# Performance work log

Measured on AMD Instinct MI355X. Metric: run time of the kernel, lower is better.

## Reference

```python
import jax, jax.numpy as jnp
import numpy as np

SEQ, B, V, E, H, L = 64, 64, 32000, 512, 512, 2


def setup_inputs() -> dict:
    key = jax.random.key(0)
    ks = jax.random.split(key, 12)
    k = float(np.sqrt(1.0 / H))
    u = lambda kk, shape, a, b: jax.random.uniform(kk, shape, jnp.float32, a, b)
    return {
        "inputs": jax.random.randint(ks[0], (SEQ, B), 0, V),          # [T, B] token ids
        "hidden": jnp.zeros((L, B, H), jnp.float32),                   # initial hidden
        "emb": u(ks[1], (V, E), -0.1, 0.1),                            # embedding table
        "Wr_w": u(ks[2], (L, H, E + H), -k, k),                        # reset gate [L,H,2H]
        "Wr_b": u(ks[3], (L, H), -k, k),
        "Wz_w": u(ks[4], (L, H, E + H), -k, k),                        # update gate
        "Wz_b": u(ks[5], (L, H), -k, k),
        "Wh_w": u(ks[6], (L, H, E + H), -k, k),                        # candidate
        "Wh_b": u(ks[7], (L, H), -k, k),
        "out_w": u(ks[8], (V, H), -0.1, 0.1),                          # output projection
        "out_b": jnp.zeros((V,), jnp.float32),
    }


def reference(inputs, hidden, emb, Wr_w, Wr_b, Wz_w, Wz_b, Wh_w, Wh_b, out_w, out_b):
    # GRU recurrence over time via lax.scan (dropout disabled: dp_keep_prob=1.0)
    def step(h, tok):
        x = emb[tok]  # [B, E]
        new_h = []
        for i in range(L):  # fixed small layer loop
            hi = h[i]  # [B, H]
            cat = jnp.concatenate([x, hi], axis=1)  # [B, E+H]
            r = jax.nn.sigmoid(cat @ Wr_w[i].T + Wr_b[i])
            z = jax.nn.sigmoid(cat @ Wz_w[i].T + Wz_b[i])
            h_hat = jnp.tanh(jnp.concatenate([x, r * hi], axis=1) @ Wh_w[i].T + Wh_b[i])
            x = (1.0 - z) * hi + z * h_hat  # next layer input / new hidden
            new_h.append(x)
        logits_t = x @ out_w.T + out_b  # [B, V]
        return jnp.stack(new_h), logits_t

    hidden_final, logits = jax.lax.scan(step, hidden, inputs)
    return logits, hidden_final  # [T,B,V], [L,B,H]
```

## Files before the change

kernel.cpp:

```cpp
#include <hip/hip_runtime.h>

constexpr int NT = 64;
constexpr int NB = 64;
constexpr int NV = 32000;
constexpr int NE = 512;
constexpr int NH = 512;
constexpr int NTILE = 32 * 250;

constexpr size_t SZ_OW  = (size_t)NV * NE;
constexpr size_t SZ_XE  = (size_t)NT * NB * NE;
constexpr size_t SZ_H   = (size_t)NB * NH;
constexpr size_t LOGITS = (size_t)NT * NB * NV;

typedef float f32x4 __attribute__((ext_vector_type(4)));
typedef int   i32x4 __attribute__((ext_vector_type(4)));
typedef short bf16x8 __attribute__((ext_vector_type(8)));
typedef short s16x4 __attribute__((ext_vector_type(4)));
typedef _Float16 f16x8 __attribute__((ext_vector_type(8)));

__device__ __forceinline__ unsigned short f2bf(float x) {
  unsigned u = __float_as_uint(x);
  u += 0x7FFFu + ((u >> 16) & 1u);
  return (unsigned short)(u >> 16);
}
__device__ __forceinline__ float bf2f(unsigned short s) {
  return __uint_as_float(((unsigned)s) << 16);
}
__device__ __forceinline__ void split2(float v, short* hi, short* lo) {
  unsigned short h = f2bf(v);
  *hi = (short)h;
  *lo = (short)f2bf(v - bf2f(h));
}
__device__ __forceinline__ f32x4 mma_bf16(bf16x8 a, bf16x8 b, f32x4 c) {
  return __builtin_amdgcn_mfma_f32_16x16x32_bf16(a, b, c, 0, 0, 0);
}
__device__ __forceinline__ f32x4 mma_f16(f16x8 a, f16x8 b, f32x4 c) {
  return __builtin_amdgcn_mfma_f32_16x16x32_f16(a, b, c, 0, 0, 0);
}

__device__ __forceinline__ void st_sc32u(unsigned* p, unsigned v) {
  asm volatile("global_store_dword %0, %1, off sc0 sc1" :: "v"(p), "v"(v) : "memory");
}
__device__ __forceinline__ void st_sc128(void* p, i32x4 v) {
  asm volatile("global_store_dwordx4 %0, %1, off sc0 sc1" :: "v"(p), "v"(v) : "memory");
}
__device__ __forceinline__ void st_nt(float* p, float v) {
  asm volatile("global_store_dword %0, %1, off nt" :: "v"(p), "v"(v) : "memory");
}
__device__ __forceinline__ unsigned ld_sc32u(const unsigned* p) {
  unsigned v;
  asm volatile("global_load_dword %0, %1, off sc0 sc1\n\ts_waitcnt vmcnt(0)"
               : "=v"(v) : "v"(p) : "memory");
  return v;
}

__device__ __forceinline__ void publish(unsigned* flags, int slot, unsigned val) {
  asm volatile("s_waitcnt vmcnt(0)" ::: "memory");
  __syncthreads();
  if (threadIdx.x == 0) st_sc32u(&flags[(size_t)slot * 32], val);
}

__global__ void k_prep(
    const float* __restrict__ outw, const int* __restrict__ toks,
    const float* __restrict__ emb, const float* __restrict__ hid,
    _Float16* OWf, short* XeHi, short* XeLo,
    short* X1Hi, short* X1Lo, short* h0Hi, short* h0Lo) {
  const size_t stride = (size_t)gridDim.x * blockDim.x;
  const size_t N1 = SZ_OW, N2 = N1 + SZ_XE, N3 = N2 + SZ_H, N4 = N3 + SZ_H;
  for (size_t x = (size_t)blockIdx.x * blockDim.x + threadIdx.x; x < N4; x += stride) {
    if (x < N1) {
      OWf[x] = (_Float16)outw[x];
    } else if (x < N2) {
      size_t p = x - N1;
      size_t r = p >> 9, c = p & 511u;
      int tok = toks[r];
      float v = emb[(size_t)tok * 512 + c];
      short hi, lo; split2(v, &hi, &lo);
      XeHi[p] = hi; XeLo[p] = lo;
    } else if (x < N3) {
      size_t p = x - N2;
      short hi, lo; split2(hid[p], &hi, &lo);
      h0Hi[p] = hi; h0Lo[p] = lo;
    } else {
      size_t p = x - N3;
      short hi, lo; split2(hid[SZ_H + p], &hi, &lo);
      X1Hi[p] = hi; X1Lo[p] = lo;
    }
  }
}

__device__ __forceinline__ void mmaP32(
    const short* __restrict__ aH, const short* __restrict__ aL, int base,
    const short* lsHi_, const short* lsLo_,
    f32x4 (&accH)[2], f32x4 (&accL)[2], int wave, int l15, int lq) {
  const int kq = wave >> 1, rhalf = wave & 1;
  const int r0 = rhalf * 16 + l15;
#pragma unroll
  for (int i = 0; i < 4; ++i) {
    const int ko = kq * 128 + i * 32 + lq * 8;
    const int kg = base + ko;
    const int e0 = (l15 * 1024 + kg) ^ ((l15 & 7) << 3);
    const int e1 = ((16 + l15) * 1024 + kg) ^ ((l15 & 7) << 3);
    bf16x8 bh0 = *(const bf16x8*)&lsHi_[e0];
    bf16x8 bl0 = *(const bf16x8*)&lsLo_[e0];
    bf16x8 bh1 = *(const bf16x8*)&lsHi_[e1];
    bf16x8 bl1 = *(const bf16x8*)&lsLo_[e1];
    bf16x8 ah = *(const bf16x8*)&aH[r0 * 512 + ko];
    bf16x8 al = *(const bf16x8*)&aL[r0 * 512 + ko];
    accH[0] = mma_bf16(ah, bh0, accH[0]);
    accH[1] = mma_bf16(ah, bh1, accH[1]);
    accL[0] = mma_bf16(al, bh0, accL[0]);
    accL[1] = mma_bf16(al, bh1, accL[1]);
    accL[0] = mma_bf16(ah, bl0, accL[0]);
    accL[1] = mma_bf16(ah, bl1, accL[1]);
  }
}
__device__ __forceinline__ void reduce4(float* lsRed_, f32x4 (&accH)[2], f32x4 (&accL)[2],
                                        f32x4 (&acc)[2], int wave, int l15, int lq) {
  const int kq = wave >> 1, rhalf = wave & 1;
  acc[0] = accH[0] + accL[0];
  acc[1] = accH[1] + accL[1];
  const int pos = l15 * 16 + lq * 4;
  if (kq) {
    *(f32x4*)&lsRed_[(((kq - 1) * 2 + rhalf) * 2 + 0) * 256 + pos] = acc[0];
    *(f32x4*)&lsRed_[(((kq - 1) * 2 + rhalf) * 2 + 1) * 256 + pos] = acc[1];
  }
  __syncthreads();
  if (!kq) {
#pragma unroll
    for (int s = 0; s < 3; ++s) {
      acc[0] += *(const f32x4*)&lsRed_[((s * 2 + rhalf) * 2 + 0) * 256 + pos];
      acc[1] += *(const f32x4*)&lsRed_[((s * 2 + rhalf) * 2 + 1) * 256 + pos];
    }
  }
  __syncthreads();
}

__device__ __forceinline__ void mmaD(
    const short* __restrict__ pAH, const short* __restrict__ pAL,
    int kloc0, int kkGlob0, const short* lsHi_, const short* lsLo_,
    f32x4 (&accH)[2], f32x4 (&accL)[2], int l15, int lq, int rhalf, int rowbase) {
  const int r0 = rowbase + rhalf * 16 + l15;
#pragma unroll 4
  for (int i = 0; i < 8; ++i) {
    const int kk = kkGlob0 + i * 32 + lq * 8;
    const int ka = kloc0 + i * 32 + lq * 8;
    const int e0 = (l15 * 1024 + kk) ^ ((l15 & 7) << 3);
    const int e1 = ((16 + l15) * 1024 + kk) ^ ((l15 & 7) << 3);
    bf16x8 bh0 = *(const bf16x8*)&lsHi_[e0];
    bf16x8 bl0 = *(const bf16x8*)&lsLo_[e0];
    bf16x8 bh1 = *(const bf16x8*)&lsHi_[e1];
    bf16x8 bl1 = *(const bf16x8*)&lsLo_[e1];
    bf16x8 ah = *(const bf16x8*)&pAH[r0 * 512 + ka];
    bf16x8 al = *(const bf16x8*)&pAL[r0 * 512 + ka];
    accH[0] = mma_bf16(ah, bh0, accH[0]);
    accH[1] = mma_bf16(ah, bh1, accH[1]);
    accL[0] = mma_bf16(al, bh0, accL[0]);
    accL[1] = mma_bf16(al, bh1, accL[1]);
    accL[0] = mma_bf16(ah, bl0, accL[0]);
    accL[1] = mma_bf16(ah, bl1, accL[1]);
  }
}
__device__ __forceinline__ void phaseD(
    const short* aLoH, const short* aLoL,
    const short* aHiH, const short* aHiL,
    const short* lsHi_, const short* lsLo_, float* lsRed_,
    f32x4 (&acc)[2], int wave, int l15, int lq, int rowbase) {
  const int khalf = wave >> 1, rhalf = wave & 1;
  f32x4 accH[2] = {}, accL[2] = {};
  const short* pAH = (khalf < 2) ? aLoH : aHiH;
  const short* pAL = (khalf < 2) ? aLoL : aHiL;
  mmaD(pAH, pAL, (khalf & 1) * 256, khalf * 256, lsHi_, lsLo_,
       accH, accL, l15, lq, rhalf, rowbase);
  acc[0] = accH[0] + accL[0];
  acc[1] = accH[1] + accL[1];
  const int pos = l15 * 16 + lq * 4;
  if (wave >= 2) {
    *(f32x4*)&lsRed_[((wave - 2) * 2 + 0) * 256 + pos] = acc[0];
    *(f32x4*)&lsRed_[((wave - 2) * 2 + 1) * 256 + pos] = acc[1];
  }
  __syncthreads();
  if (wave < 2) {
#pragma unroll
    for (int s = 0; s < 3; ++s) {
      const int slot = (wave & 1) + 2 * s;
      acc[0] += *(const f32x4*)&lsRed_[(slot * 2 + 0) * 256 + pos];
      acc[1] += *(const f32x4*)&lsRed_[(slot * 2 + 1) * 256 + pos];
    }
  }
  __syncthreads();
}

__device__ __forceinline__ void stage_weights(
    short* lsHi, short* lsLo, const float* srcBase0, const float* srcBase1,
    int jc, int tid) {
  for (int i = tid; i < 8192; i += 512) {
    const int j = i >> 8;
    const int k4 = (i & 255) << 2;
    const int g = jc + j;
    const float* src = (srcBase1 && g >= 512)
        ? (srcBase1 + (size_t)(g - 512) * 1024 + k4)
        : (srcBase0 + (size_t)g * 1024 + k4);
    f32x4 v = *(const f32x4*)src;
    s16x4 h4, l4;
#pragma unroll
    for (int q = 0; q < 4; ++q) { short hi, lo; split2(v[q], &hi, &lo); h4[q] = hi; l4[q] = lo; }
    const int els = (j * 1024 + k4) ^ ((j & 7) << 3);
    *(s16x4*)&lsHi[els] = h4;
    *(s16x4*)&lsLo[els] = l4;
  }
}

__device__ void gemm_loop(char* pool, int tid,
                          const _Float16* Af, const _Float16* Bw,
                          const float* bias, float* C,
                          unsigned* flags, unsigned* tcnt) {
  _Float16* lsA = (_Float16*)pool;
  _Float16* lsB = lsA + 128 * 64;
  volatile int* bc = (volatile int*)(pool + 32768);
  const int wave = tid >> 6, lane = tid & 63, l15 = lane & 15, lq = lane >> 4;
  const int wr = (wave >> 2) * 64, wc = (wave & 3) * 32;
  unsigned lastR = 0;
  __syncthreads();
  for (;;) {
    if (tid == 0)
      *bc = (int)__hip_atomic_fetch_add(tcnt, 1u, __ATOMIC_RELAXED,
                                        __HIP_MEMORY_SCOPE_AGENT);
    __syncthreads();
    const int tau = *bc;
    __syncthreads();
    if (tau >= NTILE) break;
    const int bm = tau / 250, bn = tau - bm * 250;
    const unsigned Rneed = 2u * (unsigned)bm + 2u;
    if (lastR < Rneed) {
      if (tid < 32) {
        const unsigned* fp = &flags[(size_t)(160 + tid) * 32];
        while (ld_sc32u(fp) < Rneed) __builtin_amdgcn_s_sleep(8);
      }
      lastR = Rneed;
    }
    __syncthreads();
    f32x4 acc[4][2] = {};
    const size_t arow0 = (size_t)bm * 128;
    const size_t brow0 = (size_t)bn * 128;
    for (int kb = 0; kb < 512; kb += 64) {
#pragma unroll
      for (int i = 0; i < 2; ++i) {
        int c = tid + i * 512;
        int row = c >> 3, kc = (c & 7) * 8;
        f16x8 va = *(const f16x8*)(Af + (arow0 + row) * 512 + kb + kc);
        f16x8 vb = *(const f16x8*)(Bw + (brow0 + row) * 512 + kb + kc);
        int el = (row * 64 + kc) ^ ((row & 7) << 3);
        *(f16x8*)&lsA[el] = va;
        *(f16x8*)&lsB[el] = vb;
      }
      __syncthreads();
#pragma unroll
      for (int k0 = 0; k0 < 64; k0 += 32) {
        const int kk = k0 + lq * 8;
        f16x8 af[4], bfr[2];
#pragma unroll
        for (int i = 0; i < 4; ++i) {
          int ra = wr + i * 16 + l15;
          af[i] = *(const f16x8*)&lsA[(ra * 64 + kk) ^ ((ra & 7) << 3)];
        }
#pragma unroll
        for (int jt = 0; jt < 2; ++jt) {
          int rb = wc + jt * 16 + l15;
          bfr[jt] = *(const f16x8*)&lsB[(rb * 64 + kk) ^ ((rb & 7) << 3)];
        }
#pragma unroll
        for (int i = 0; i < 4; ++i)
#pragma unroll
          for (int jt = 0; jt < 2; ++jt)
            acc[i][jt] = mma_f16(af[i], bfr[jt], acc[i][jt]);
      }
      __syncthreads();
    }
#pragma unroll
    for (int i = 0; i < 4; ++i) {
#pragma unroll
      for (int jt = 0; jt < 2; ++jt) {
        const size_t col = brow0 + wc + jt * 16 + l15;
        const float bval = bias[col];
#pragma unroll
        for (int r = 0; r < 4; ++r) {
          const size_t row = arow0 + wr + i * 16 + lq * 4 + r;
          st_nt(&C[row * (size_t)NV + col], acc[i][jt][r] + bval);
        }
      }
    }
  }
}

__launch_bounds__(512, 1)
__global__ void k_main(
    const float* __restrict__ Wr, const float* __restrict__ Wz, const float* __restrict__ Wh,
    const float* __restrict__ Wrb, const float* __restrict__ Wzb, const float* __restrict__ Whb,
    const short* __restrict__ XeHi, const short* __restrict__ XeLo,
    short* X1Hi, short* X1Lo, _Float16* X1f16,
    short* h0Hi, short* h0Lo,
    short* rh0Hi, short* rh0Lo, short* rh1Hi, short* rh1Lo,
    float* z0, float* z1, float* hidOut,
    const _Float16* OWf, const float* outb, float* out,
    unsigned* flags, unsigned* tcnt) {
  __shared__ __align__(16) char pool[153600];
  short* lsHi = (short*)pool;
  short* lsLo = lsHi + 32 * 1024;
  float* lsRed = (float*)(pool + 131072);
  short* sH    = (short*)(pool + 131072);
  short* sL    = sH + 1024;
  float* sZA   = (float*)(pool + 131072);
  short* stH   = (short*)(pool + 143360);
  short* stL   = stH + 1024;
  float* sZ    = (float*)(pool + 147456);
  _Float16* sX = (_Float16*)(pool + 151552);

  const int wg = blockIdx.x;
  const int tid = threadIdx.x;
  const int wave = tid >> 6, lane = tid & 63, l15 = lane & 15, lq = lane >> 4;

  if (wg < 64) {
    const int cg = wg >> 1, rh = wg & 1, jc = cg * 32, rowbase = rh * 32;
    const bool isR = (jc < 512);
    stage_weights(lsHi, lsLo, Wr, Wz, jc, tid);
    float biasL0, biasL1;
    {
      const int j0 = jc + l15, j1 = j0 + 16;
      biasL0 = (j0 < 512) ? Wrb[j0] : Wzb[j0 - 512];
      biasL1 = (j1 < 512) ? Wrb[j1] : Wzb[j1 - 512];
    }
    __syncthreads();
    for (int t = 0; t < NT; ++t) {
      f32x4 accH[2] = {}, accL[2] = {};
      mmaP32(XeHi + (size_t)t * SZ_H + rowbase * 512,
             XeLo + (size_t)t * SZ_H + rowbase * 512, 0,
             lsHi, lsLo, accH, accL, wave, l15, lq);
      if (tid < 16) {
        const unsigned* fp = &flags[(size_t)(128 + tid * 2 + rh) * 32];
        while (ld_sc32u(fp) < (unsigned)t) {}
      }
      __syncthreads();
      const short* hH = h0Hi + (size_t)t * SZ_H + rowbase * 512;
      const short* hL = h0Lo + (size_t)t * SZ_H + rowbase * 512;
      if (isR && tid < 256) {
        const int buf = tid >> 7, q = tid & 127, row = q >> 2, c = q & 3;
        *(i32x4*)&(buf ? stL : stH)[row * 32 + c * 8] =
            *(const i32x4*)((buf ? hL : hH) + row * 512 + jc + c * 8);
      }
      mmaP32(hH, hL, 512, lsHi, lsLo, accH, accL, wave, l15, lq);
      f32x4 acc[2];
      reduce4(lsRed, accH, accL, acc, wave, l15, lq);
      if (wave < 2) {
#pragma unroll
        for (int ct = 0; ct < 2; ++ct) {
          const int jj = ct * 16 + l15;
          const float bv = ct ? biasL1 : biasL0;
#pragma unroll
          for (int r = 0; r < 4; ++r) {
            const int lb = wave * 16 + lq * 4 + r;
            const float s = 1.0f / (1.0f + __expf(-(acc[ct][r] + bv)));
            if (isR) {
              const float hv = bf2f((unsigned short)stH[lb * 32 + jj]) +
                               bf2f((unsigned short)stL[lb * 32 + jj]);
              short hi, lo; split2(s * hv, &hi, &lo);
              sH[lb * 32 + jj] = hi; sL[lb * 32 + jj] = lo;
            } else {
              sZA[lb * 32 + jj] = s;
            }
          }
        }
      }
      __syncthreads();
      if (isR) {
        if (tid < 256) {
          const int buf = tid >> 7, q = tid & 127, row = q >> 2, c = q & 3;
          i32x4 v = *(const i32x4*)&(buf ? sL : sH)[row * 32 + c * 8];
          st_sc128((buf ? rh0Lo : rh0Hi) + (size_t)t * SZ_H +
                   (size_t)(rowbase + row) * 512 + jc + c * 8, v);
        }
      } else {
        if (tid < 256) {
          const int row = tid >> 3, c = tid & 7;
          i32x4 v = *(const i32x4*)&sZA[row * 32 + c * 4];
          st_sc128(z0 + (size_t)t * SZ_H + (size_t)(rowbase + row) * 512 +
                   (jc - 512) + c * 4, v);
        }
      }
      publish(flags, wg, (unsigned)(t + 1));
    }
  } else if (wg < 128) {
    const int idx = wg - 64, cg = idx >> 1, rh = idx & 1, jc = cg * 32, rowbase = rh * 32;
    const bool isR = (jc < 512);
    stage_weights(lsHi, lsLo, Wr + (size_t)512 * 1024, Wz + (size_t)512 * 1024, jc, tid);
    float biasL0, biasL1;
    {
      const int j0 = jc + l15, j1 = j0 + 16;
      biasL0 = (j0 < 512) ? Wrb[512 + j0] : Wzb[512 + j0 - 512];
      biasL1 = (j1 < 512) ? Wrb[512 + j1] : Wzb[512 + j1 - 512];
    }
    __syncthreads();
    for (int t = 0; t < NT; ++t) {
      if (tid < 16) {
        const unsigned* fp = &flags[(size_t)(128 + tid * 2 + rh) * 32];
        while (ld_sc32u(fp) < (unsigned)(t + 1)) {}
      } else if (tid >= 64 && tid < 80) {
        const unsigned* fp = &flags[(size_t)(160 + (tid - 64) * 2 + rh) * 32];
        while (ld_sc32u(fp) < (unsigned)t) {}
      }
      __syncthreads();
      const short* xH = h0Hi + (size_t)(t + 1) * SZ_H;
      const short* xL = h0Lo + (size_t)(t + 1) * SZ_H;
      const short* hH = X1Hi + (size_t)t * SZ_H;
      const short* hL = X1Lo + (size_t)t * SZ_H;
      if (isR && tid < 256) {
        const int buf = tid >> 7, q = tid & 127, row = q >> 2, c = q & 3;
        *(i32x4*)&(buf ? stL : stH)[row * 32 + c * 8] =
            *(const i32x4*)((buf ? hL : hH) + (size_t)(rowbase + row) * 512 + jc + c * 8);
      }
      f32x4 acc[2];
      phaseD(xH, xL, hH, hL, lsHi, lsLo, lsRed, acc, wave, l15, lq, rowbase);
      if (wave < 2) {
#pragma unroll
        for (int ct = 0; ct < 2; ++ct) {
          const int jj = ct * 16 + l15;
          const float bv = ct ? biasL1 : biasL0;
#pragma unroll
          for (int r = 0; r < 4; ++r) {
            const int lb = wave * 16 + lq * 4 + r;
            const float s = 1.0f / (1.0f + __expf(-(acc[ct][r] + bv)));
            if (isR) {
              const float hv = bf2f((unsigned short)stH[lb * 32 + jj]) +
                               bf2f((unsigned short)stL[lb * 32 + jj]);
              short hi, lo; split2(s * hv, &hi, &lo);
              sH[lb * 32 + jj] = hi; sL[lb * 32 + jj] = lo;
            } else {
              sZA[lb * 32 + jj] = s;
            }
          }
        }
      }
      __syncthreads();
      if (isR) {
        if (tid < 256) {
          const int buf = tid >> 7, q = tid & 127, row = q >> 2, c = q & 3;
          i32x4 v = *(const i32x4*)&(buf ? sL : sH)[row * 32 + c * 8];
          st_sc128((buf ? rh1Lo : rh1Hi) + (size_t)t * SZ_H +
                   (size_t)(rowbase + row) * 512 + jc + c * 8, v);
        }
      } else {
        if (tid < 256) {
          const int row = tid >> 3, c = tid & 7;
          i32x4 v = *(const i32x4*)&sZA[row * 32 + c * 4];
          st_sc128(z1 + (size_t)t * SZ_H + (size_t)(rowbase + row) * 512 +
                   (jc - 512) + c * 4, v);
        }
      }
      publish(flags, wg, (unsigned)(t + 1));
    }
  } else if (wg < 192) {
    const bool isL1 = (wg >= 160);
    const int idx = isL1 ? (wg - 160) : (wg - 128);
    const int cg = idx >> 1, rh = idx & 1, jc = cg * 32, rowbase = rh * 32;
    const int layer = isL1 ? 1 : 0;
    stage_weights(lsHi, lsLo, Wh + (size_t)layer * 512 * 1024, nullptr, jc, tid);
    const float biasL0 = Whb[layer * 512 + jc + l15];
    const float biasL1 = Whb[layer * 512 + jc + 16 + l15];
    __syncthreads();
    short* myHi = isL1 ? X1Hi : h0Hi;
    short* myLo = isL1 ? X1Lo : h0Lo;
    const short* rhHi_ = isL1 ? rh1Hi : rh0Hi;
    const short* rhLo_ = isL1 ? rh1Lo : rh0Lo;
    const float* zArr = isL1 ? z1 : z0;
    for (int t = 0; t < NT; ++t) {
      if (tid < 256) {
        const int buf = tid >> 7, q = tid & 127, row = q >> 2, c = q & 3;
        const short* src = (buf ? myLo : myHi) + (size_t)t * SZ_H +
                           (size_t)(rowbase + row) * 512 + jc + c * 8;
        *(i32x4*)&(buf ? stL : stH)[row * 32 + c * 8] = *(const i32x4*)src;
      }
      if (isL1) {
        if (tid < 16) {
          const unsigned* fp = &flags[(size_t)(128 + tid * 2 + rh) * 32];
          while (ld_sc32u(fp) < (unsigned)(t + 1)) {}
        }
        __syncthreads();
      }
      f32x4 accH[2] = {}, accL[2] = {};
      if (isL1) {
        mmaP32(h0Hi + (size_t)(t + 1) * SZ_H + rowbase * 512,
               h0Lo + (size_t)(t + 1) * SZ_H + rowbase * 512, 0,
               lsHi, lsLo, accH, accL, wave, l15, lq);
      } else {
        mmaP32(XeHi + (size_t)t * SZ_H + rowbase * 512,
               XeLo + (size_t)t * SZ_H + rowbase * 512, 0,
               lsHi, lsLo, accH, accL, wave, l15, lq);
      }
      if (tid < 32) {
        const int base = isL1 ? 64 : 0;
        const unsigned* fp = &flags[(size_t)(base + tid * 2 + rh) * 32];
        while (ld_sc32u(fp) < (unsigned)(t + 1)) {}
      }
      __syncthreads();
      if (tid < 256) {
        const int row = tid >> 3, c = tid & 7;
        *(f32x4*)&sZ[row * 32 + c * 4] =
            *(const f32x4*)(zArr + (size_t)t * SZ_H + (size_t)(rowbase + row) * 512 +
                            jc + c * 4);
      }
      mmaP32(rhHi_ + (size_t)t * SZ_H + rowbase * 512,
             rhLo_ + (size_t)t * SZ_H + rowbase * 512, 512,
             lsHi, lsLo, accH, accL, wave, l15, lq);
      f32x4 acc[2];
      reduce4(lsRed, accH, accL, acc, wave, l15, lq);
      if (wave < 2) {
#pragma unroll
        for (int ct = 0; ct < 2; ++ct) {
          const int jj = ct * 16 + l15, j = jc + jj;
          const float bv = ct ? biasL1 : biasL0;
#pragma unroll
          for (int r = 0; r < 4; ++r) {
            const int lb = wave * 16 + lq * 4 + r;
            const float hh = tanhf(acc[ct][r] + bv);
            const float z = sZ[lb * 32 + jj];
            const float ho = bf2f((unsigned short)stH[lb * 32 + jj]) +
                             bf2f((unsigned short)stL[lb * 32 + jj]);
            const float hn = (1.0f - z) * ho + z * hh;
            short hi, lo; split2(hn, &hi, &lo);
            sH[lb * 32 + jj] = hi; sL[lb * 32 + jj] = lo;
            if (isL1) sX[lb * 32 + jj] = (_Float16)hn;
            if (t == NT - 1)
              hidOut[(size_t)layer * SZ_H + (size_t)(rowbase + lb) * 512 + j] = hn;
          }
        }
      }
      __syncthreads();
      if (tid < 256) {
        const int buf = tid >> 7, q = tid & 127, row = q >> 2, c = q & 3;
        i32x4 v = *(const i32x4*)&(buf ? sL : sH)[row * 32 + c * 8];
        st_sc128((buf ? myLo : myHi) + (size_t)(t + 1) * SZ_H +
                 (size_t)(rowbase + row) * 512 + jc + c * 8, v);
      } else if (isL1 && tid < 384) {
        const int q = tid - 256, row = q >> 2, c = q & 3;
        i32x4 v = *(const i32x4*)&sX[row * 32 + c * 8];
        st_sc128(X1f16 + (size_t)t * SZ_H + (size_t)(rowbase + row) * 512 + jc + c * 8, v);
      }
      publish(flags, wg, (unsigned)(t + 1));
    }
  }
  {
    unsigned* tc = tcnt;
    gemm_loop(pool, tid, X1f16, OWf, outb, out, flags, tc);
  }
}

extern "C" void kernel_launch(void* const* d_in, const int* in_sizes, int n_in,
                              void* d_out, int out_size, void* d_ws, size_t ws_size,
                              hipStream_t stream) {
  (void)in_sizes; (void)n_in; (void)out_size; (void)ws_size;
  const int*   toks = (const int*)d_in[0];
  const float* hid  = (const float*)d_in[1];
  const float* emb  = (const float*)d_in[2];
  const float* Wr   = (const float*)d_in[3];
  const float* Wrb  = (const float*)d_in[4];
  const float* Wz   = (const float*)d_in[5];
  const float* Wzb  = (const float*)d_in[6];
  const float* Wh   = (const float*)d_in[7];
  const float* Whb  = (const float*)d_in[8];
  const float* outw = (const float*)d_in[9];
  const float* outb = (const float*)d_in[10];
  float* out = (float*)d_out;

  char* base = (char*)d_ws;
  size_t off = 0;
  auto carve = [&](size_t bytes) -> char* {
    char* r = base + off;
    off = (off + bytes + 255) & ~(size_t)255;
    return r;
  };
  _Float16* OWf   = (_Float16*)carve(SZ_OW * 2);
  short*    XeHi  = (short*)carve(SZ_XE * 2);
  short*    XeLo  = (short*)carve(SZ_XE * 2);
  short*    X1Hi  = (short*)carve((size_t)(NT + 1) * SZ_H * 2);
  short*    X1Lo  = (short*)carve((size_t)(NT + 1) * SZ_H * 2);
  _Float16* X1f16 = (_Float16*)carve((size_t)NT * SZ_H * 2);
  short*    h0Hi  = (short*)carve((size_t)(NT + 1) * SZ_H * 2);
  short*    h0Lo  = (short*)carve((size_t)(NT + 1) * SZ_H * 2);
  short*    rh0Hi = (short*)carve((size_t)NT * SZ_H * 2);
  short*    rh0Lo = (short*)carve((size_t)NT * SZ_H * 2);
  short*    rh1Hi = (short*)carve((size_t)NT * SZ_H * 2);
  short*    rh1Lo = (short*)carve((size_t)NT * SZ_H * 2);
  float*    z0    = (float*)carve((size_t)NT * SZ_H * 4);
  float*    z1    = (float*)carve((size_t)NT * SZ_H * 4);
  unsigned* flags = (unsigned*)carve(32768);
  unsigned* tcnt  = (unsigned*)carve(256);

  hipMemsetAsync(flags, 0, 32768, stream);
  hipMemsetAsync(tcnt, 0, 256, stream);

  k_prep<<<2048, 256, 0, stream>>>(outw, toks, emb, hid,
                                   OWf, XeHi, XeLo, X1Hi, X1Lo, h0Hi, h0Lo);

  k_main<<<256, 512, 0, stream>>>(
      Wr, Wz, Wh, Wrb, Wzb, Whb, XeHi, XeLo,
      X1Hi, X1Lo, X1f16, h0Hi, h0Lo,
      rh0Hi, rh0Lo, rh1Hi, rh1Lo, z0, z1,
      out + LOGITS, OWf, outb, out, flags, tcnt);
}
```

Before: 790.9 us.

## Pair GEMM tiles along M, prefetch recurrent loads into registers, use fast activations

The output-projection GEMM now processes two 128-row A tiles per work item, reusing each loaded B (out_w) tile for 256 rows. This halves B traffic and the number of atomic tile fetches, but doubles accumulator registers and waits for more recurrence progress before starting. Global loads of hidden state and z in the recurrent phases are now issued into registers before the MFMA loop and written to LDS afterward, to hide their latency. Sigmoid and tanh now use an rcp-based fast approximation, which trades some precision for fewer instructions.

```diff
diff --git a/kernel.cpp b/kernel.cpp
--- a/kernel.cpp
+++ b/kernel.cpp
@@ -5,7 +5,7 @@
 constexpr int NV = 32000;
 constexpr int NE = 512;
 constexpr int NH = 512;
-constexpr int NTILE = 32 * 250;
+constexpr int NPAIR = 16 * 250;
 
 constexpr size_t SZ_OW  = (size_t)NV * NE;
 constexpr size_t SZ_XE  = (size_t)NT * NB * NE;
@@ -36,6 +36,12 @@
 }
 __device__ __forceinline__ f32x4 mma_f16(f16x8 a, f16x8 b, f32x4 c) {
   return __builtin_amdgcn_mfma_f32_16x16x32_f16(a, b, c, 0, 0, 0);
+}
+__device__ __forceinline__ float fast_sigmoid(float x) {
+  return __builtin_amdgcn_rcpf(1.0f + __expf(-x));
+}
+__device__ __forceinline__ float fast_tanh(float x) {
+  return 1.0f - 2.0f * __builtin_amdgcn_rcpf(1.0f + __expf(2.0f * x));
 }
 
 __device__ __forceinline__ void st_sc32u(unsigned* p, unsigned v) {
@@ -215,9 +221,10 @@
                           const _Float16* Af, const _Float16* Bw,
                           const float* bias, float* C,
                           unsigned* flags, unsigned* tcnt) {
-  _Float16* lsA = (_Float16*)pool;
-  _Float16* lsB = lsA + 128 * 64;
-  volatile int* bc = (volatile int*)(pool + 32768);
+  _Float16* lsA0 = (_Float16*)pool;
+  _Float16* lsA1 = lsA0 + 128 * 64;
+  _Float16* lsB  = lsA1 + 128 * 64;
+  volatile int* bc = (volatile int*)(pool + 49152);
   const int wave = tid >> 6, lane = tid & 63, l15 = lane & 15, lq = lane >> 4;
   const int wr = (wave >> 2) * 64, wc = (wave & 3) * 32;
   unsigned lastR = 0;
@@ -227,11 +234,11 @@
       *bc = (int)__hip_atomic_fetch_add(tcnt, 1u, __ATOMIC_RELAXED,
                                         __HIP_MEMORY_SCOPE_AGENT);
     __syncthreads();
-    const int tau = *bc;
+    const int pr = *bc;
     __syncthreads();
-    if (tau >= NTILE) break;
-    const int bm = tau / 250, bn = tau - bm * 250;
-    const unsigned Rneed = 2u * (unsigned)bm + 2u;
+    if (pr >= NPAIR) break;
+    const int p = pr / 250, bn = pr - p * 250;
+    const unsigned Rneed = 4u * (unsigned)p + 4u;
     if (lastR < Rneed) {
       if (tid < 32) {
         const unsigned* fp = &flags[(size_t)(160 + tid) * 32];
@@ -240,29 +247,30 @@
       lastR = Rneed;
     }
     __syncthreads();
-    f32x4 acc[4][2] = {};
-    const size_t arow0 = (size_t)bm * 128;
+    f32x4 acc0[4][2] = {}, acc1[4][2] = {};
+    const size_t arow0 = (size_t)p * 256;
     const size_t brow0 = (size_t)bn * 128;
     for (int kb = 0; kb < 512; kb += 64) {
 #pragma unroll
       for (int i = 0; i < 2; ++i) {
         int c = tid + i * 512;
         int row = c >> 3, kc = (c & 7) * 8;
-        f16x8 va = *(const f16x8*)(Af + (arow0 + row) * 512 + kb + kc);
-        f16x8 vb = *(const f16x8*)(Bw + (brow0 + row) * 512 + kb + kc);
         int el = (row * 64 + kc) ^ ((row & 7) << 3);
-        *(f16x8*)&lsA[el] = va;
-        *(f16x8*)&lsB[el] = vb;
+        *(f16x8*)&lsA0[el] = *(const f16x8*)(Af + (arow0 + row) * 512 + kb + kc);
+        *(f16x8*)&lsA1[el] = *(const f16x8*)(Af + (arow0 + 128 + row) * 512 + kb + kc);
+        *(f16x8*)&lsB[el]  = *(const f16x8*)(Bw + (brow0 + row) * 512 + kb + kc);
       }
       __syncthreads();
 #pragma unroll
       for (int k0 = 0; k0 < 64; k0 += 32) {
         const int kk = k0 + lq * 8;
-        f16x8 af[4], bfr[2];
+        f16x8 af0[4], af1[4], bfr[2];
 #pragma unroll
         for (int i = 0; i < 4; ++i) {
           int ra = wr + i * 16 + l15;
-          af[i] = *(const f16x8*)&lsA[(ra * 64 + kk) ^ ((ra & 7) << 3)];
+          int el = (ra * 64 + kk) ^ ((ra & 7) << 3);
+          af0[i] = *(const f16x8*)&lsA0[el];
+          af1[i] = *(const f16x8*)&lsA1[el];
         }
 #pragma unroll
         for (int jt = 0; jt < 2; ++jt) {
@@ -272,8 +280,10 @@
 #pragma unroll
         for (int i = 0; i < 4; ++i)
 #pragma unroll
-          for (int jt = 0; jt < 2; ++jt)
-            acc[i][jt] = mma_f16(af[i], bfr[jt], acc[i][jt]);
+          for (int jt = 0; jt < 2; ++jt) {
+            acc0[i][jt] = mma_f16(af0[i], bfr[jt], acc0[i][jt]);
+            acc1[i][jt] = mma_f16(af1[i], bfr[jt], acc1[i][jt]);
+          }
       }
       __syncthreads();
     }
@@ -286,7 +296,8 @@
 #pragma unroll
         for (int r = 0; r < 4; ++r) {
           const size_t row = arow0 + wr + i * 16 + lq * 4 + r;
-          st_nt(&C[row * (size_t)NV + col], acc[i][jt][r] + bval);
+          st_nt(&C[row * (size_t)NV + col], acc0[i][jt][r] + bval);
+          st_nt(&C[(row + 128) * (size_t)NV + col], acc1[i][jt][r] + bval);
         }
       }
     }
@@ -343,12 +354,13 @@
       __syncthreads();
       const short* hH = h0Hi + (size_t)t * SZ_H + rowbase * 512;
       const short* hL = h0Lo + (size_t)t * SZ_H + rowbase * 512;
-      if (isR && tid < 256) {
-        const int buf = tid >> 7, q = tid & 127, row = q >> 2, c = q & 3;
-        *(i32x4*)&(buf ? stL : stH)[row * 32 + c * 8] =
-            *(const i32x4*)((buf ? hL : hH) + row * 512 + jc + c * 8);
-      }
+      i32x4 pre;
+      const int pbuf = tid >> 7, pq = tid & 127, prow = pq >> 2, pc = pq & 3;
+      if (isR && tid < 256)
+        pre = *(const i32x4*)((pbuf ? hL : hH) + prow * 512 + jc + pc * 8);
       mmaP32(hH, hL, 512, lsHi, lsLo, accH, accL, wave, l15, lq);
+      if (isR && tid < 256)
+        *(i32x4*)&(pbuf ? stL : stH)[prow * 32 + pc * 8] = pre;
       f32x4 acc[2];
       reduce4(lsRed, accH, accL, acc, wave, l15, lq);
       if (wave < 2) {
@@ -359,7 +371,7 @@
 #pragma unroll
           for (int r = 0; r < 4; ++r) {
             const int lb = wave * 16 + lq * 4 + r;
-            const float s = 1.0f / (1.0f + __expf(-(acc[ct][r] + bv)));
+            const float s = fast_sigmoid(acc[ct][r] + bv);
             if (isR) {
               const float hv = bf2f((unsigned short)stH[lb * 32 + jj]) +
                                bf2f((unsigned short)stL[lb * 32 + jj]);
@@ -374,10 +386,9 @@
       __syncthreads();
       if (isR) {
         if (tid < 256) {
-          const int buf = tid >> 7, q = tid & 127, row = q >> 2, c = q & 3;
-          i32x4 v = *(const i32x4*)&(buf ? sL : sH)[row * 32 + c * 8];
-          st_sc128((buf ? rh0Lo : rh0Hi) + (size_t)t * SZ_H +
-                   (size_t)(rowbase + row) * 512 + jc + c * 8, v);
+          i32x4 v = *(const i32x4*)&(pbuf ? sL : sH)[prow * 32 + pc * 8];
+          st_sc128((pbuf ? rh0Lo : rh0Hi) + (size_t)t * SZ_H +
+                   (size_t)(rowbase + prow) * 512 + jc + pc * 8, v);
         }
       } else {
         if (tid < 256) {
@@ -413,13 +424,16 @@
       const short* xL = h0Lo + (size_t)(t + 1) * SZ_H;
       const short* hH = X1Hi + (size_t)t * SZ_H;
       const short* hL = X1Lo + (size_t)t * SZ_H;
-      if (isR && tid < 256) {
-        const int buf = tid >> 7, q = tid & 127, row = q >> 2, c = q & 3;
-        *(i32x4*)&(buf ? stL : stH)[row * 32 + c * 8] =
-            *(const i32x4*)((buf ? hL : hH) + (size_t)(rowbase + row) * 512 + jc + c * 8);
-      }
+      i32x4 pre;
+      const int pbuf = tid >> 7, pq = tid & 127, prow = pq >> 2, pc = pq & 3;
+      if (isR && tid < 256)
+        pre = *(const i32x4*)((pbuf ? hL : hH) +
+                              (size_t)(rowbase + prow) * 512 + jc + pc * 8);
       f32x4 acc[2];
       phaseD(xH, xL, hH, hL, lsHi, lsLo, lsRed, acc, wave, l15, lq, rowbase);
+      if (isR && tid < 256)
+        *(i32x4*)&(pbuf ? stL : stH)[prow * 32 + pc * 8] = pre;
+      __syncthreads();
       if (wave < 2) {
 #pragma unroll
         for (int ct = 0; ct < 2; ++ct) {
@@ -428,7 +442,7 @@
 #pragma unroll
           for (int r = 0; r < 4; ++r) {
             const int lb = wave * 16 + lq * 4 + r;
-            const float s = 1.0f / (1.0f + __expf(-(acc[ct][r] + bv)));
+            const float s = fast_sigmoid(acc[ct][r] + bv);
             if (isR) {
               const float hv = bf2f((unsigned short)stH[lb * 32 + jj]) +
                                bf2f((unsigned short)stL[lb * 32 + jj]);
@@ -443,10 +457,9 @@
       __syncthreads();
       if (isR) {
         if (tid < 256) {
-          const int buf = tid >> 7, q = tid & 127, row = q >> 2, c = q & 3;
-          i32x4 v = *(const i32x4*)&(buf ? sL : sH)[row * 32 + c * 8];
-          st_sc128((buf ? rh1Lo : rh1Hi) + (size_t)t * SZ_H +
-                   (size_t)(rowbase + row) * 512 + jc + c * 8, v);
+          i32x4 v = *(const i32x4*)&(pbuf ? sL : sH)[prow * 32 + pc * 8];
+          st_sc128((pbuf ? rh1Lo : rh1Hi) + (size_t)t * SZ_H +
+                   (size_t)(rowbase + prow) * 512 + jc + pc * 8, v);
         }
       } else {
         if (tid < 256) {
@@ -472,22 +485,21 @@
     const short* rhHi_ = isL1 ? rh1Hi : rh0Hi;
     const short* rhLo_ = isL1 ? rh1Lo : rh0Lo;
     const float* zArr = isL1 ? z1 : z0;
+    const int fbase = isL1 ? 64 : 0;
     for (int t = 0; t < NT; ++t) {
+      const int pbuf = tid >> 7, pq = tid & 127, prow = pq >> 2, pc = pq & 3;
       if (tid < 256) {
-        const int buf = tid >> 7, q = tid & 127, row = q >> 2, c = q & 3;
-        const short* src = (buf ? myLo : myHi) + (size_t)t * SZ_H +
-                           (size_t)(rowbase + row) * 512 + jc + c * 8;
-        *(i32x4*)&(buf ? stL : stH)[row * 32 + c * 8] = *(const i32x4*)src;
-      }
+        const short* src = (pbuf ? myLo : myHi) + (size_t)t * SZ_H +
+                           (size_t)(rowbase + prow) * 512 + jc + pc * 8;
+        *(i32x4*)&(pbuf ? stL : stH)[prow * 32 + pc * 8] = *(const i32x4*)src;
+      }
+      f32x4 accH[2] = {}, accL[2] = {};
       if (isL1) {
         if (tid < 16) {
           const unsigned* fp = &flags[(size_t)(128 + tid * 2 + rh) * 32];
           while (ld_sc32u(fp) < (unsigned)(t + 1)) {}
         }
         __syncthreads();
-      }
-      f32x4 accH[2] = {}, accL[2] = {};
-      if (isL1) {
         mmaP32(h0Hi + (size_t)(t + 1) * SZ_H + rowbase * 512,
                h0Lo + (size_t)(t + 1) * SZ_H + rowbase * 512, 0,
                lsHi, lsLo, accH, accL, wave, l15, lq);
@@ -497,20 +509,20 @@
                lsHi, lsLo, accH, accL, wave, l15, lq);
       }
       if (tid < 32) {
-        const int base = isL1 ? 64 : 0;
-        const unsigned* fp = &flags[(size_t)(base + tid * 2 + rh) * 32];
+        const unsigned* fp = &flags[(size_t)(fbase + tid * 2 + rh) * 32];
         while (ld_sc32u(fp) < (unsigned)(t + 1)) {}
       }
       __syncthreads();
-      if (tid < 256) {
-        const int row = tid >> 3, c = tid & 7;
-        *(f32x4*)&sZ[row * 32 + c * 4] =
-            *(const f32x4*)(zArr + (size_t)t * SZ_H + (size_t)(rowbase + row) * 512 +
-                            jc + c * 4);
-      }
+      f32x4 zv;
+      const int zrow = tid >> 3, zc = tid & 7;
+      if (tid < 256)
+        zv = *(const f32x4*)(zArr + (size_t)t * SZ_H +
+                             (size_t)(rowbase + zrow) * 512 + jc + zc * 4);
       mmaP32(rhHi_ + (size_t)t * SZ_H + rowbase * 512,
              rhLo_ + (size_t)t * SZ_H + rowbase * 512, 512,
              lsHi, lsLo, accH, accL, wave, l15, lq);
+      if (tid < 256)
+        *(f32x4*)&sZ[zrow * 32 + zc * 4] = zv;
       f32x4 acc[2];
       reduce4(lsRed, accH, accL, acc, wave, l15, lq);
       if (wave < 2) {
@@ -521,7 +533,7 @@
 #pragma unroll
           for (int r = 0; r < 4; ++r) {
             const int lb = wave * 16 + lq * 4 + r;
-            const float hh = tanhf(acc[ct][r] + bv);
+            const float hh = fast_tanh(acc[ct][r] + bv);
             const float z = sZ[lb * 32 + jj];
             const float ho = bf2f((unsigned short)stH[lb * 32 + jj]) +
                              bf2f((unsigned short)stL[lb * 32 + jj]);
@@ -536,10 +548,9 @@
       }
       __syncthreads();
       if (tid < 256) {
-        const int buf = tid >> 7, q = tid & 127, row = q >> 2, c = q & 3;
-        i32x4 v = *(const i32x4*)&(buf ? sL : sH)[row * 32 + c * 8];
-        st_sc128((buf ? myLo : myHi) + (size_t)(t + 1) * SZ_H +
-                 (size_t)(rowbase + row) * 512 + jc + c * 8, v);
+        i32x4 v = *(const i32x4*)&(pbuf ? sL : sH)[prow * 32 + pc * 8];
+        st_sc128((pbuf ? myLo : myHi) + (size_t)(t + 1) * SZ_H +
+                 (size_t)(rowbase + prow) * 512 + jc + pc * 8, v);
       } else if (isL1 && tid < 384) {
         const int q = tid - 256, row = q >> 2, c = q & 3;
         i32x4 v = *(const i32x4*)&sX[row * 32 + c * 8];
@@ -548,10 +559,7 @@
       publish(flags, wg, (unsigned)(t + 1));
     }
   }
-  {
-    unsigned* tc = tcnt;
-    gemm_loop(pool, tid, X1f16, OWf, outb, out, flags, tc);
-  }
+  gemm_loop(pool, tid, X1f16, OWf, outb, out, flags, tcnt);
 }
 
 extern "C" void kernel_launch(void* const* d_in, const int* in_sizes, int n_in,
```

Result: faster. 724.8 us (-8.4%).
